# Kernel tuning notes

Hardware: AMD Instinct MI355X
Metric: run time of the kernel (lower is better)

## Reference

```python
import jax, jax.numpy as jnp
import numpy as np

B, NP, PS, D = 4, 512, 16, 1024
NH = 4            # intra attention heads
HD = D // NH      # intra head dim
PH = 4            # pool heads
PHD = D // PH     # pool head dim
K = 5             # depthwise conv kernel size


def _rms_norm(x):
    # F.rms_norm with eps=None -> eps = finfo(dtype).eps, no learned weight
    eps = jnp.finfo(x.dtype).eps
    return x * jax.lax.rsqrt(jnp.mean(x * x, axis=-1, keepdims=True) + eps)


def setup_inputs() -> dict:
    key = jax.random.key(0)
    ks = jax.random.split(key, 12)
    s = 0.02
    return {
        "patch_byte_emb": jax.random.normal(ks[0], (B, NP, PS, D), jnp.float32),
        "local_pos": jax.random.normal(ks[1], (PS, D), jnp.float32) * 0.01,
        "w_gate": jax.random.normal(ks[2], (D, D), jnp.float32) * s,
        "w_in": jax.random.normal(ks[3], (D, D), jnp.float32) * s,
        "conv_w": jax.random.normal(ks[4], (D, 1, K), jnp.float32) * s,  # depthwise (out=D, in/groups=1, k)
        "w_qkv": jax.random.normal(ks[5], (3 * D, D), jnp.float32) * s,
        "w_intra_out": jax.random.normal(ks[6], (D, D), jnp.float32) * s,
        "w_pool": jax.random.normal(ks[7], (PH, D), jnp.float32) * s,
        "attn_temperature": jnp.ones((1,), jnp.float32),
        "w_up": jax.random.normal(ks[8], (D, D), jnp.float32) * s,
        "w_down": jax.random.normal(ks[9], (D, D), jnp.float32) * s,
        "w_out": jax.random.normal(ks[10], (D, D), jnp.float32) * s,
    }


def reference(patch_byte_emb, local_pos, w_gate, w_in, conv_w, w_qkv,
              w_intra_out, w_pool, attn_temperature, w_up, w_down, w_out):
    x = patch_byte_emb + local_pos[None, None]            # [B,NP,PS,D]
    x = _rms_norm(x)
    # SiLU-gated projection (CastedLinear: y = x @ W.T, no bias)
    x = jax.nn.silu(x @ w_gate.T) * (x @ w_in.T)
    bsz, num_patches, patch_size, model_dim = x.shape

    # depthwise causal-style conv1d: padding=4 both sides, then keep first PS outputs
    x_flat = x.reshape(bsz * num_patches, patch_size, model_dim).transpose(0, 2, 1)  # [BN,D,PS]
    conv_out = jax.lax.conv_general_dilated(
        x_flat, conv_w, window_strides=(1,), padding=[(K - 1, K - 1)],
        feature_group_count=model_dim,
        dimension_numbers=("NCH", "OIH", "NCH"))[:, :, :patch_size]
    x = x + conv_out.transpose(0, 2, 1).reshape(bsz, num_patches, patch_size, model_dim)

    # tiny per-patch self-attention
    x_sa = _rms_norm(x).reshape(bsz * num_patches, patch_size, model_dim)
    qkv = (x_sa @ w_qkv.T).reshape(bsz * num_patches, patch_size, 3, NH, HD)
    q, k, v = qkv[:, :, 0], qkv[:, :, 1], qkv[:, :, 2]    # [BN,PS,NH,HD]
    attn = jnp.einsum("bqhd,bkhd->bhqk", q, k) * (HD ** -0.5)
    attn = jax.nn.softmax(attn, axis=-1)
    sa = jnp.einsum("bhqk,bkhd->bqhd", attn, v).reshape(bsz * num_patches, patch_size, model_dim)
    x = x + (sa @ w_intra_out.T).reshape(bsz, num_patches, patch_size, model_dim)

    # multi-head attention pooling over patch positions
    x = _rms_norm(x)
    temp = jnp.clip(attn_temperature, 0.01, None).astype(x.dtype)  # [1]
    attn_logits = (x @ w_pool.T) / temp                   # [B,NP,PS,PH]
    attn_w = jax.nn.softmax(attn_logits.transpose(0, 1, 3, 2), axis=-1)  # [B,NP,PH,PS]
    x_heads = x.reshape(bsz, num_patches, patch_size, PH, PHD)
    pooled = jnp.einsum("bnhp,bnphd->bnhd", attn_w, x_heads).reshape(bsz, num_patches, model_dim)

    # post MLP + out proj
    y = pooled + (jax.nn.silu(_rms_norm(pooled) @ w_up.T) @ w_down.T)
    y = y @ w_out.T
    return _rms_norm(y)
```

## Files before the change

### kernel.cpp

```cpp
#include <hip/hip_runtime.h>
#include <cstdint>
#include <cstddef>


typedef __bf16 bf16x8 __attribute__((ext_vector_type(8)));
typedef float floatx4 __attribute__((ext_vector_type(4)));

#define DEV static __device__ __forceinline__

DEV unsigned short f2bf(float f) {
  union { float f; unsigned u; } x; x.f = f;
  unsigned r = x.u + 0x7fffu + ((x.u >> 16) & 1u);
  return (unsigned short)(r >> 16);
}
DEV float bf2f(unsigned short b) {
  union { unsigned u; float f; } x; x.u = ((unsigned)b) << 16;
  return x.f;
}
DEV float silu_f(float v) { return v / (1.f + __expf(-v)); }

DEV void gl_lds16(const unsigned short* g, unsigned short* l) {
  __builtin_amdgcn_global_load_lds(
      (const __attribute__((address_space(1))) void*)g,
      (__attribute__((address_space(3))) void*)l, 16, 0, 0);
}

DEV float block_reduce_sum(float v) {
  #pragma unroll
  for (int o = 32; o > 0; o >>= 1) v += __shfl_down(v, o, 64);
  __shared__ float s[4];
  int w = threadIdx.x >> 6;
  if ((threadIdx.x & 63) == 0) s[w] = v;
  __syncthreads();
  return s[0] + s[1] + s[2] + s[3];
}

struct CvtArgs {
  const float* src[7];
  unsigned short* dst[7];
  int blkoff[8];
};
__global__ __launch_bounds__(256) void cvt_all(CvtArgs a) {
  int b = blockIdx.x;
  int w = 0;
  #pragma unroll
  for (int i = 0; i < 6; i++) w += (b >= a.blkoff[i + 1]) ? 1 : 0;
  int i = (b - a.blkoff[w]) * 1024 + threadIdx.x * 4;
  float4 v = *(const float4*)(a.src[w] + i);
  ushort4 o;
  o.x = f2bf(v.x); o.y = f2bf(v.y); o.z = f2bf(v.z); o.w = f2bf(v.w);
  *(ushort4*)(a.dst[w] + i) = o;
}

__global__ __launch_bounds__(256) void prep_kernel(const float* __restrict__ pbe,
                                                   const float* __restrict__ pos,
                                                   unsigned short* __restrict__ xn) {
  int row = blockIdx.x;
  int t = row & 15;
  const float* ip = pbe + (size_t)row * 1024;
  const float* pp = pos + (size_t)t * 1024;
  int c = threadIdx.x * 4;
  float4 v = *(const float4*)(ip + c);
  float4 p = *(const float4*)(pp + c);
  v.x += p.x; v.y += p.y; v.z += p.z; v.w += p.w;
  float ss = v.x * v.x + v.y * v.y + v.z * v.z + v.w * v.w;
  ss = block_reduce_sum(ss);
  float sc = rsqrtf(ss * (1.f / 1024.f) + 1.1920929e-7f);
  ushort4 o;
  o.x = f2bf(v.x * sc); o.y = f2bf(v.y * sc); o.z = f2bf(v.z * sc); o.w = f2bf(v.w * sc);
  *(ushort4*)(xn + (size_t)row * 1024 + c) = o;
}

DEV float ldval(const float* p, size_t i) { return p[i]; }
DEV float ldval(const unsigned short* p, size_t i) { return bf2f(p[i]); }
DEV void stval(float* p, size_t i, float v) { p[i] = v; }
DEV void stval(unsigned short* p, size_t i, float v) { p[i] = f2bf(v); }

template <typename TI, typename TO>
__global__ __launch_bounds__(256) void rmsnorm_kernel(const TI* __restrict__ in,
                                                      TO* __restrict__ out) {
  size_t row = blockIdx.x;
  const TI* ip = in + row * 1024;
  TO* op = out + row * 1024;
  int c = threadIdx.x * 4;
  float v[4]; float ss = 0.f;
  #pragma unroll
  for (int j = 0; j < 4; j++) { v[j] = ldval(ip, c + j); ss += v[j] * v[j]; }
  ss = block_reduce_sum(ss);
  float sc = rsqrtf(ss * (1.f / 1024.f) + 1.1920929e-7f);
  #pragma unroll
  for (int j = 0; j < 4; j++) stval(op, c + j, v[j] * sc);
}


DEV void stage_tile(const unsigned short* __restrict__ src, size_t ld,
                    unsigned short* lds, int wave, int lane, int k0) {
  int r0 = wave * 32 + (lane >> 2);
  int r1 = r0 + 16;
  int c0 = (lane & 3) ^ ((r0 >> 1) & 3);
  int c1 = (lane & 3) ^ ((r1 >> 1) & 3);
  gl_lds16(src + (size_t)r0 * ld + k0 + c0 * 8, lds + wave * 1024);
  gl_lds16(src + (size_t)r1 * ld + k0 + c1 * 8, lds + wave * 1024 + 512);
}
DEV void stage_tile64(const unsigned short* __restrict__ src, size_t ld,
                      unsigned short* lds, int wave, int lane, int k0) {
  int r = wave * 16 + (lane >> 2);
  int c = (lane & 3) ^ ((r >> 1) & 3);
  gl_lds16(src + (size_t)r * ld + k0 + c * 8, lds + wave * 512);
}
DEV int frag_off(int row, int quad) {
  return row * 32 + ((quad ^ ((row >> 1) & 3)) * 8);
}

template <int EPI>
__global__ __launch_bounds__(256) void gemm_bt(
    const unsigned short* __restrict__ A, const unsigned short* __restrict__ Bw,
    int M, int N, int K,
    float* __restrict__ outF, unsigned short* __restrict__ outB,
    const unsigned short* __restrict__ resB, const float* __restrict__ resF) {
  __shared__ __align__(16) unsigned short As[128 * 32];
  __shared__ __align__(16) unsigned short Bs[128 * 32];
  const int tid = threadIdx.x;
  const int bm = blockIdx.y * 128, bn = blockIdx.x * 128;
  const int wave = tid >> 6, lane = tid & 63;
  const int wy = wave >> 1, wx = wave & 1;
  const int l15 = lane & 15, quad = lane >> 4;

  floatx4 acc[4][4];
  #pragma unroll
  for (int i = 0; i < 4; i++)
    #pragma unroll
    for (int j = 0; j < 4; j++)
      #pragma unroll
      for (int r = 0; r < 4; r++) acc[i][j][r] = 0.f;

  const unsigned short* Ab = A + (size_t)bm * K;
  const unsigned short* Bb = Bw + (size_t)bn * K;
  int aoff[4], boff[4];
  #pragma unroll
  for (int i = 0; i < 4; i++) {
    aoff[i] = frag_off(wy * 64 + i * 16 + l15, quad);
    boff[i] = frag_off(wx * 64 + i * 16 + l15, quad);
  }

  for (int k0 = 0; k0 < K; k0 += 32) {
    __syncthreads();
    stage_tile(Ab, K, As, wave, lane, k0);
    stage_tile(Bb, K, Bs, wave, lane, k0);
    __syncthreads();
    bf16x8 afr[4], bfr[4];
    #pragma unroll
    for (int i = 0; i < 4; i++) afr[i] = *(const bf16x8*)&As[aoff[i]];
    #pragma unroll
    for (int j = 0; j < 4; j++) bfr[j] = *(const bf16x8*)&Bs[boff[j]];
    #pragma unroll
    for (int i = 0; i < 4; i++)
      #pragma unroll
      for (int j = 0; j < 4; j++)
        acc[i][j] = __builtin_amdgcn_mfma_f32_16x16x32_bf16(afr[i], bfr[j], acc[i][j], 0, 0, 0);
  }

  #pragma unroll
  for (int i = 0; i < 4; i++)
    #pragma unroll
    for (int j = 0; j < 4; j++) {
      int gm = bm + wy * 64 + i * 16 + quad * 4;
      int gn = bn + wx * 64 + j * 16 + l15;
      #pragma unroll
      for (int r = 0; r < 4; r++) {
        float v = acc[i][j][r];
        size_t idx = (size_t)(gm + r) * N + gn;
        if (EPI == 0) outF[idx] = v;
        else if (EPI == 1) outB[idx] = f2bf(v);
        else if (EPI == 2) outB[idx] = f2bf(silu_f(v));
        else if (EPI == 3) outB[idx] = f2bf(v + bf2f(resB[idx]));
        else if (EPI == 4) outB[idx] = f2bf(v + resF[idx]);
      }
    }
}

__global__ __launch_bounds__(256, 2) void gemm_dual(
    const unsigned short* __restrict__ A, const unsigned short* __restrict__ Bg,
    const unsigned short* __restrict__ Bi, int M, int N, int K,
    unsigned short* __restrict__ outH) {
  __shared__ __align__(16) unsigned short As[128 * 32];
  __shared__ __align__(16) unsigned short Gs[64 * 32];
  __shared__ __align__(16) unsigned short Is[64 * 32];
  const int tid = threadIdx.x;
  const int bm = blockIdx.y * 128, bn = blockIdx.x * 64;
  const int wave = tid >> 6, lane = tid & 63;
  const int wy = wave >> 1, wx = wave & 1;
  const int l15 = lane & 15, quad = lane >> 4;

  floatx4 accg[4][2], acci[4][2];
  #pragma unroll
  for (int i = 0; i < 4; i++)
    #pragma unroll
    for (int j = 0; j < 2; j++)
      #pragma unroll
      for (int r = 0; r < 4; r++) { accg[i][j][r] = 0.f; acci[i][j][r] = 0.f; }

  const unsigned short* Ab = A + (size_t)bm * K;
  const unsigned short* Gb = Bg + (size_t)bn * K;
  const unsigned short* Ib = Bi + (size_t)bn * K;
  int aoff[4], boff[2];
  #pragma unroll
  for (int i = 0; i < 4; i++) aoff[i] = frag_off(wy * 64 + i * 16 + l15, quad);
  #pragma unroll
  for (int j = 0; j < 2; j++) boff[j] = frag_off(wx * 32 + j * 16 + l15, quad);

  for (int k0 = 0; k0 < K; k0 += 32) {
    __syncthreads();
    stage_tile(Ab, K, As, wave, lane, k0);
    stage_tile64(Gb, K, Gs, wave, lane, k0);
    stage_tile64(Ib, K, Is, wave, lane, k0);
    __syncthreads();
    bf16x8 afr[4], gfr[2], ifr[2];
    #pragma unroll
    for (int i = 0; i < 4; i++) afr[i] = *(const bf16x8*)&As[aoff[i]];
    #pragma unroll
    for (int j = 0; j < 2; j++) {
      gfr[j] = *(const bf16x8*)&Gs[boff[j]];
      ifr[j] = *(const bf16x8*)&Is[boff[j]];
    }
    #pragma unroll
    for (int i = 0; i < 4; i++)
      #pragma unroll
      for (int j = 0; j < 2; j++) {
        accg[i][j] = __builtin_amdgcn_mfma_f32_16x16x32_bf16(afr[i], gfr[j], accg[i][j], 0, 0, 0);
        acci[i][j] = __builtin_amdgcn_mfma_f32_16x16x32_bf16(afr[i], ifr[j], acci[i][j], 0, 0, 0);
      }
  }

  #pragma unroll
  for (int i = 0; i < 4; i++)
    #pragma unroll
    for (int j = 0; j < 2; j++) {
      int gm = bm + wy * 64 + i * 16 + quad * 4;
      int gn = bn + wx * 32 + j * 16 + l15;
      #pragma unroll
      for (int r = 0; r < 4; r++) {
        size_t idx = (size_t)(gm + r) * N + gn;
        outH[idx] = f2bf(silu_f(accg[i][j][r]) * acci[i][j][r]);
      }
    }
}

__global__ __launch_bounds__(256) void conv_rms_kernel(const unsigned short* __restrict__ h,
                                                       const float* __restrict__ cw,
                                                       unsigned short* __restrict__ x2,
                                                       unsigned short* __restrict__ x2n) {
  int patch = blockIdx.x;
  __shared__ __align__(16) unsigned short hs[16 * 1024];
  __shared__ __align__(16) float cws[5120];
  const int tid = threadIdx.x;
  size_t base = (size_t)patch * 16384;
  for (int idx = tid * 8; idx < 16384; idx += 256 * 8)
    *(uint4*)&hs[idx] = *(const uint4*)&h[base + idx];
  for (int i = tid * 4; i < 5120; i += 256 * 4)
    *(float4*)&cws[i] = *(const float4*)&cw[i];
  __syncthreads();
  int t = tid >> 4;
  int lc = (tid & 15) * 8;
  float vals[8][8];
  float ss = 0.f;
  #pragma unroll
  for (int jb = 0; jb < 8; jb++) {
    #pragma unroll
    for (int i = 0; i < 8; i++) {
      int c = jb * 128 + lc + i;
      float acc = bf2f(hs[t * 1024 + c]);
      #pragma unroll
      for (int k = 0; k < 5; k++) {
        int tt = t + k - 4;
        if (tt >= 0) acc += cws[c * 5 + k] * bf2f(hs[tt * 1024 + c]);
      }
      vals[jb][i] = acc;
      ss += acc * acc;
    }
  }
  ss += __shfl_down(ss, 8, 16);
  ss += __shfl_down(ss, 4, 16);
  ss += __shfl_down(ss, 2, 16);
  ss += __shfl_down(ss, 1, 16);
  ss = __shfl(ss, 0, 16);
  float sc = rsqrtf(ss * (1.f / 1024.f) + 1.1920929e-7f);
  #pragma unroll
  for (int jb = 0; jb < 8; jb++) {
    ushort4 o2[2], on[2];
    #pragma unroll
    for (int i = 0; i < 8; i++) {
      ((unsigned short*)o2)[i] = f2bf(vals[jb][i]);
      ((unsigned short*)on)[i] = f2bf(vals[jb][i] * sc);
    }
    size_t off = base + (size_t)t * 1024 + jb * 128 + lc;
    *(uint4*)&x2[off] = *(uint4*)o2;
    *(uint4*)&x2n[off] = *(uint4*)on;
  }
}

__global__ __launch_bounds__(256) void attn_kernel(const unsigned short* __restrict__ qkv,
                                                   unsigned short* __restrict__ sa) {
  int patch = blockIdx.x;
  int head = blockIdx.y;
  const int tid = threadIdx.x;
  __shared__ float qs[16][260], ks[16][260], vs[16][260];
  __shared__ float sc[16][16];
  size_t base = (size_t)patch * 16 * 3072 + (size_t)head * 256;
  for (int idx = tid * 8; idx < 16 * 256; idx += 256 * 8) {
    int t = idx >> 8, d = idx & 255;
    size_t roff = base + (size_t)t * 3072 + d;
    uint4 qv = *(const uint4*)&qkv[roff];
    uint4 kv = *(const uint4*)&qkv[roff + 1024];
    uint4 vv = *(const uint4*)&qkv[roff + 2048];
    const unsigned short* qp = (const unsigned short*)&qv;
    const unsigned short* kp = (const unsigned short*)&kv;
    const unsigned short* vp = (const unsigned short*)&vv;
    #pragma unroll
    for (int i = 0; i < 8; i++) {
      qs[t][d + i] = bf2f(qp[i]);
      ks[t][d + i] = bf2f(kp[i]);
      vs[t][d + i] = bf2f(vp[i]);
    }
  }
  __syncthreads();
  {
    int t = tid >> 4, kk = tid & 15;
    float s = 0.f;
    for (int d = 0; d < 256; d++) s += qs[t][d] * ks[kk][d];
    sc[t][kk] = s * 0.0625f;
  }
  __syncthreads();
  if (tid < 16) {
    float m = -1e30f;
    for (int kk = 0; kk < 16; kk++) m = fmaxf(m, sc[tid][kk]);
    float p[16], sum = 0.f;
    for (int kk = 0; kk < 16; kk++) { p[kk] = __expf(sc[tid][kk] - m); sum += p[kk]; }
    float inv = 1.f / sum;
    for (int kk = 0; kk < 16; kk++) sc[tid][kk] = p[kk] * inv;
  }
  __syncthreads();
  for (int idx = tid * 8; idx < 4096; idx += 256 * 8) {
    int t = idx >> 8, d = idx & 255;
    ushort4 o[2];
    #pragma unroll
    for (int i = 0; i < 8; i++) {
      float v = 0.f;
      #pragma unroll
      for (int kk = 0; kk < 16; kk++) v += sc[t][kk] * vs[kk][d + i];
      ((unsigned short*)o)[i] = f2bf(v);
    }
    *(uint4*)&sa[(size_t)(patch * 16 + t) * 1024 + head * 256 + d] = *(uint4*)o;
  }
}

__global__ __launch_bounds__(256) void pool_kernel(const unsigned short* __restrict__ x4,
                                                   const float* __restrict__ wpool,
                                                   const float* __restrict__ tptr,
                                                   float* __restrict__ pooled) {
  int patch = blockIdx.x;
  __shared__ __align__(16) unsigned short xs[16 * 1024];
  __shared__ float lg[4][16], aw[4][16];
  const int tid = threadIdx.x;
  size_t base = (size_t)patch * 16384;
  for (int idx = tid * 8; idx < 16384; idx += 256 * 8)
    *(uint4*)&xs[idx] = *(const uint4*)&x4[base + idx];
  __syncthreads();
  {
    int pair = tid >> 2, sub = tid & 3;
    int t = pair >> 2, hh = pair & 3;
    float s = 0.f;
    for (int d = sub * 256; d < sub * 256 + 256; d++)
      s += bf2f(xs[t * 1024 + d]) * wpool[hh * 1024 + d];
    s += __shfl_down(s, 2, 64);
    s += __shfl_down(s, 1, 64);
    if (sub == 0) {
      float temp = fmaxf(tptr[0], 0.01f);
      lg[hh][t] = s / temp;
    }
  }
  __syncthreads();
  if (tid < 4) {
    int hh = tid;
    float m = -1e30f;
    for (int t = 0; t < 16; t++) m = fmaxf(m, lg[hh][t]);
    float p[16], sum = 0.f;
    for (int t = 0; t < 16; t++) { p[t] = __expf(lg[hh][t] - m); sum += p[t]; }
    float inv = 1.f / sum;
    for (int t = 0; t < 16; t++) aw[hh][t] = p[t] * inv;
  }
  __syncthreads();
  for (int c = tid; c < 1024; c += 256) {
    int hh = c >> 8;
    float o = 0.f;
    #pragma unroll
    for (int t = 0; t < 16; t++) o += aw[hh][t] * bf2f(xs[t * 1024 + c]);
    pooled[(size_t)patch * 1024 + c] = o;
  }
}

extern "C" void kernel_launch(void* const* d_in, const int* in_sizes, int n_in,
                              void* d_out, int out_size, void* d_ws, size_t ws_size,
                              hipStream_t stream) {
  (void)in_sizes; (void)n_in; (void)out_size; (void)ws_size;
  const float* pbe  = (const float*)d_in[0];
  const float* lpos = (const float*)d_in[1];
  const float* wg   = (const float*)d_in[2];
  const float* wi   = (const float*)d_in[3];
  const float* cw   = (const float*)d_in[4];
  const float* wqkv = (const float*)d_in[5];
  const float* wio  = (const float*)d_in[6];
  const float* wpl  = (const float*)d_in[7];
  const float* temp = (const float*)d_in[8];
  const float* wup  = (const float*)d_in[9];
  const float* wdn  = (const float*)d_in[10];
  const float* wout = (const float*)d_in[11];
  float* outp = (float*)d_out;

  const int ROWS = 32768, Dm = 1024, NPAT = 2048;

  char* p = (char*)d_ws;
  auto take = [&](size_t nbytes) { void* r = (void*)p; p += (nbytes + 255) & ~(size_t)255; return r; };
  unsigned short* wg_b   = (unsigned short*)take((size_t)Dm * Dm * 2);
  unsigned short* wi_b   = (unsigned short*)take((size_t)Dm * Dm * 2);
  unsigned short* wqkv_b = (unsigned short*)take((size_t)3 * Dm * Dm * 2);
  unsigned short* wio_b  = (unsigned short*)take((size_t)Dm * Dm * 2);
  unsigned short* wup_b  = (unsigned short*)take((size_t)Dm * Dm * 2);
  unsigned short* wdn_b  = (unsigned short*)take((size_t)Dm * Dm * 2);
  unsigned short* wout_b = (unsigned short*)take((size_t)Dm * Dm * 2);
  unsigned short* slotA  = (unsigned short*)take((size_t)ROWS * Dm * 2);
  unsigned short* slotB  = (unsigned short*)take((size_t)ROWS * Dm * 2);
  unsigned short* slotC  = (unsigned short*)take((size_t)ROWS * Dm * 2);
  unsigned short* qkvB   = (unsigned short*)take((size_t)ROWS * 3 * Dm * 2);
  float*          pooled = (float*)take((size_t)NPAT * Dm * 4);
  unsigned short* pooledn= (unsigned short*)take((size_t)NPAT * Dm * 2);
  unsigned short* ubuf   = (unsigned short*)take((size_t)NPAT * Dm * 2);
  unsigned short* y1b    = (unsigned short*)take((size_t)NPAT * Dm * 2);
  float*          y2     = (float*)take((size_t)NPAT * Dm * 4);

  CvtArgs ca;
  ca.src[0] = wg;   ca.dst[0] = wg_b;
  ca.src[1] = wi;   ca.dst[1] = wi_b;
  ca.src[2] = wqkv; ca.dst[2] = wqkv_b;
  ca.src[3] = wio;  ca.dst[3] = wio_b;
  ca.src[4] = wup;  ca.dst[4] = wup_b;
  ca.src[5] = wdn;  ca.dst[5] = wdn_b;
  ca.src[6] = wout; ca.dst[6] = wout_b;
  int off = 0;
  for (int i = 0; i < 7; i++) { ca.blkoff[i] = off; off += (i == 2) ? 3072 : 1024; }
  ca.blkoff[7] = off;
  cvt_all<<<dim3(off), dim3(256), 0, stream>>>(ca);

  prep_kernel<<<dim3(ROWS), dim3(256), 0, stream>>>(pbe, lpos, slotA);
  gemm_dual<<<dim3(Dm / 64, ROWS / 128), dim3(256), 0, stream>>>(
      slotA, wg_b, wi_b, ROWS, Dm, Dm, slotB);
  conv_rms_kernel<<<dim3(NPAT), dim3(256), 0, stream>>>(slotB, cw, slotC, slotA);
  gemm_bt<1><<<dim3(3 * Dm / 128, ROWS / 128), dim3(256), 0, stream>>>(
      slotA, wqkv_b, ROWS, 3 * Dm, Dm, nullptr, qkvB, nullptr, nullptr);
  attn_kernel<<<dim3(NPAT, 4), dim3(256), 0, stream>>>(qkvB, slotB);
  gemm_bt<3><<<dim3(Dm / 128, ROWS / 128), dim3(256), 0, stream>>>(
      slotB, wio_b, ROWS, Dm, Dm, nullptr, slotC, slotC, nullptr);
  rmsnorm_kernel<unsigned short, unsigned short><<<dim3(ROWS), dim3(256), 0, stream>>>(slotC, slotA);
  pool_kernel<<<dim3(NPAT), dim3(256), 0, stream>>>(slotA, wpl, temp, pooled);
  rmsnorm_kernel<float, unsigned short><<<dim3(NPAT), dim3(256), 0, stream>>>(pooled, pooledn);
  gemm_bt<2><<<dim3(Dm / 128, NPAT / 128), dim3(256), 0, stream>>>(
      pooledn, wup_b, NPAT, Dm, Dm, nullptr, ubuf, nullptr, nullptr);
  gemm_bt<4><<<dim3(Dm / 128, NPAT / 128), dim3(256), 0, stream>>>(
      ubuf, wdn_b, NPAT, Dm, Dm, nullptr, y1b, nullptr, pooled);
  gemm_bt<0><<<dim3(Dm / 128, NPAT / 128), dim3(256), 0, stream>>>(
      y1b, wout_b, NPAT, Dm, Dm, y2, nullptr, nullptr, nullptr);
  rmsnorm_kernel<float, float><<<dim3(NPAT), dim3(256), 0, stream>>>(y2, outp);
}
```

Baseline: 1.179 ms.

## Deepen GEMM K-tiles to 64, vectorize conv/attention, fuse pooled rmsnorm

```diff
diff --git a/kernel.cpp b/kernel.cpp
--- a/kernel.cpp
+++ b/kernel.cpp
@@ -93,79 +93,80 @@
 }
 
 
-DEV void stage_tile(const unsigned short* __restrict__ src, size_t ld,
-                    unsigned short* lds, int wave, int lane, int k0) {
-  int r0 = wave * 32 + (lane >> 2);
-  int r1 = r0 + 16;
-  int c0 = (lane & 3) ^ ((r0 >> 1) & 3);
-  int c1 = (lane & 3) ^ ((r1 >> 1) & 3);
-  gl_lds16(src + (size_t)r0 * ld + k0 + c0 * 8, lds + wave * 1024);
-  gl_lds16(src + (size_t)r1 * ld + k0 + c1 * 8, lds + wave * 1024 + 512);
-}
-DEV void stage_tile64(const unsigned short* __restrict__ src, size_t ld,
-                      unsigned short* lds, int wave, int lane, int k0) {
-  int r = wave * 16 + (lane >> 2);
-  int c = (lane & 3) ^ ((r >> 1) & 3);
-  gl_lds16(src + (size_t)r * ld + k0 + c * 8, lds + wave * 512);
-}
-DEV int frag_off(int row, int quad) {
-  return row * 32 + ((quad ^ ((row >> 1) & 3)) * 8);
-}
-
-template <int EPI>
+template <int R>
+DEV void stage_rows(const unsigned short* __restrict__ src, int ldK,
+                    unsigned short* lds, int k0, int wave, int lane) {
+  constexpr int PER_WAVE = R / 32;
+  #pragma unroll
+  for (int d = 0; d < PER_WAVE; d++) {
+    int di = wave * PER_WAVE + d;
+    int r = di * 8 + (lane >> 3);
+    int c = (lane & 7) ^ (r & 7);
+    gl_lds16(src + (size_t)r * ldK + k0 + c * 8, lds + di * 512);
+  }
+}
+DEV int frag_off64(int row, int g) {
+  return row * 64 + ((g ^ (row & 7)) * 8);
+}
+
+template <int EPI, int TM, int TN>
 __global__ __launch_bounds__(256) void gemm_bt(
     const unsigned short* __restrict__ A, const unsigned short* __restrict__ Bw,
     int M, int N, int K,
     float* __restrict__ outF, unsigned short* __restrict__ outB,
     const unsigned short* __restrict__ resB, const float* __restrict__ resF) {
-  __shared__ __align__(16) unsigned short As[128 * 32];
-  __shared__ __align__(16) unsigned short Bs[128 * 32];
+  constexpr int AI = TM / 32;
+  constexpr int BJ = TN / 32;
+  __shared__ __align__(16) unsigned short As[TM * 64];
+  __shared__ __align__(16) unsigned short Bs[TN * 64];
   const int tid = threadIdx.x;
-  const int bm = blockIdx.y * 128, bn = blockIdx.x * 128;
+  const int bm = blockIdx.y * TM, bn = blockIdx.x * TN;
   const int wave = tid >> 6, lane = tid & 63;
   const int wy = wave >> 1, wx = wave & 1;
   const int l15 = lane & 15, quad = lane >> 4;
 
-  floatx4 acc[4][4];
-  #pragma unroll
-  for (int i = 0; i < 4; i++)
-    #pragma unroll
-    for (int j = 0; j < 4; j++)
+  floatx4 acc[AI][BJ];
+  #pragma unroll
+  for (int i = 0; i < AI; i++)
+    #pragma unroll
+    for (int j = 0; j < BJ; j++)
       #pragma unroll
       for (int r = 0; r < 4; r++) acc[i][j][r] = 0.f;
 
   const unsigned short* Ab = A + (size_t)bm * K;
   const unsigned short* Bb = Bw + (size_t)bn * K;
-  int aoff[4], boff[4];
-  #pragma unroll
-  for (int i = 0; i < 4; i++) {
-    aoff[i] = frag_off(wy * 64 + i * 16 + l15, quad);
-    boff[i] = frag_off(wx * 64 + i * 16 + l15, quad);
-  }
-
-  for (int k0 = 0; k0 < K; k0 += 32) {
+  int arow[AI], brow[BJ];
+  #pragma unroll
+  for (int i = 0; i < AI; i++) arow[i] = wy * (TM / 2) + i * 16 + l15;
+  #pragma unroll
+  for (int j = 0; j < BJ; j++) brow[j] = wx * (TN / 2) + j * 16 + l15;
+
+  for (int k0 = 0; k0 < K; k0 += 64) {
     __syncthreads();
-    stage_tile(Ab, K, As, wave, lane, k0);
-    stage_tile(Bb, K, Bs, wave, lane, k0);
+    stage_rows<TM>(Ab, K, As, k0, wave, lane);
+    stage_rows<TN>(Bb, K, Bs, k0, wave, lane);
     __syncthreads();
-    bf16x8 afr[4], bfr[4];
-    #pragma unroll
-    for (int i = 0; i < 4; i++) afr[i] = *(const bf16x8*)&As[aoff[i]];
-    #pragma unroll
-    for (int j = 0; j < 4; j++) bfr[j] = *(const bf16x8*)&Bs[boff[j]];
-    #pragma unroll
-    for (int i = 0; i < 4; i++)
-      #pragma unroll
-      for (int j = 0; j < 4; j++)
-        acc[i][j] = __builtin_amdgcn_mfma_f32_16x16x32_bf16(afr[i], bfr[j], acc[i][j], 0, 0, 0);
-  }
-
-  #pragma unroll
-  for (int i = 0; i < 4; i++)
-    #pragma unroll
-    for (int j = 0; j < 4; j++) {
-      int gm = bm + wy * 64 + i * 16 + quad * 4;
-      int gn = bn + wx * 64 + j * 16 + l15;
+    #pragma unroll
+    for (int h = 0; h < 2; h++) {
+      bf16x8 afr[AI], bfr[BJ];
+      #pragma unroll
+      for (int i = 0; i < AI; i++) afr[i] = *(const bf16x8*)&As[frag_off64(arow[i], h * 4 + quad)];
+      #pragma unroll
+      for (int j = 0; j < BJ; j++) bfr[j] = *(const bf16x8*)&Bs[frag_off64(brow[j], h * 4 + quad)];
+      #pragma unroll
+      for (int i = 0; i < AI; i++)
+        #pragma unroll
+        for (int j = 0; j < BJ; j++)
+          acc[i][j] = __builtin_amdgcn_mfma_f32_16x16x32_bf16(afr[i], bfr[j], acc[i][j], 0, 0, 0);
+    }
+  }
+
+  #pragma unroll
+  for (int i = 0; i < AI; i++)
+    #pragma unroll
+    for (int j = 0; j < BJ; j++) {
+      int gm = bm + wy * (TM / 2) + i * 16 + quad * 4;
+      int gn = bn + wx * (TN / 2) + j * 16 + l15;
       #pragma unroll
       for (int r = 0; r < 4; r++) {
         float v = acc[i][j][r];
@@ -179,13 +180,13 @@
     }
 }
 
-__global__ __launch_bounds__(256, 2) void gemm_dual(
+__global__ __launch_bounds__(256) void gemm_dual(
     const unsigned short* __restrict__ A, const unsigned short* __restrict__ Bg,
     const unsigned short* __restrict__ Bi, int M, int N, int K,
     unsigned short* __restrict__ outH) {
-  __shared__ __align__(16) unsigned short As[128 * 32];
-  __shared__ __align__(16) unsigned short Gs[64 * 32];
-  __shared__ __align__(16) unsigned short Is[64 * 32];
+  __shared__ __align__(16) unsigned short As[128 * 64];
+  __shared__ __align__(16) unsigned short Gs[64 * 64];
+  __shared__ __align__(16) unsigned short Is[64 * 64];
   const int tid = threadIdx.x;
   const int bm = blockIdx.y * 128, bn = blockIdx.x * 64;
   const int wave = tid >> 6, lane = tid & 63;
@@ -203,33 +204,36 @@
   const unsigned short* Ab = A + (size_t)bm * K;
   const unsigned short* Gb = Bg + (size_t)bn * K;
   const unsigned short* Ib = Bi + (size_t)bn * K;
-  int aoff[4], boff[2];
-  #pragma unroll
-  for (int i = 0; i < 4; i++) aoff[i] = frag_off(wy * 64 + i * 16 + l15, quad);
-  #pragma unroll
-  for (int j = 0; j < 2; j++) boff[j] = frag_off(wx * 32 + j * 16 + l15, quad);
-
-  for (int k0 = 0; k0 < K; k0 += 32) {
+  int arow[4], brow[2];
+  #pragma unroll
+  for (int i = 0; i < 4; i++) arow[i] = wy * 64 + i * 16 + l15;
+  #pragma unroll
+  for (int j = 0; j < 2; j++) brow[j] = wx * 32 + j * 16 + l15;
+
+  for (int k0 = 0; k0 < K; k0 += 64) {
     __syncthreads();
-    stage_tile(Ab, K, As, wave, lane, k0);
-    stage_tile64(Gb, K, Gs, wave, lane, k0);
-    stage_tile64(Ib, K, Is, wave, lane, k0);
+    stage_rows<128>(Ab, K, As, k0, wave, lane);
+    stage_rows<64>(Gb, K, Gs, k0, wave, lane);
+    stage_rows<64>(Ib, K, Is, k0, wave, lane);
     __syncthreads();
-    bf16x8 afr[4], gfr[2], ifr[2];
-    #pragma unroll
-    for (int i = 0; i < 4; i++) afr[i] = *(const bf16x8*)&As[aoff[i]];
-    #pragma unroll
-    for (int j = 0; j < 2; j++) {
-      gfr[j] = *(const bf16x8*)&Gs[boff[j]];
-      ifr[j] = *(const bf16x8*)&Is[boff[j]];
-    }
-    #pragma unroll
-    for (int i = 0; i < 4; i++)
+    #pragma unroll
+    for (int h = 0; h < 2; h++) {
+      bf16x8 afr[4], gfr[2], ifr[2];
+      #pragma unroll
+      for (int i = 0; i < 4; i++) afr[i] = *(const bf16x8*)&As[frag_off64(arow[i], h * 4 + quad)];
       #pragma unroll
       for (int j = 0; j < 2; j++) {
-        accg[i][j] = __builtin_amdgcn_mfma_f32_16x16x32_bf16(afr[i], gfr[j], accg[i][j], 0, 0, 0);
-        acci[i][j] = __builtin_amdgcn_mfma_f32_16x16x32_bf16(afr[i], ifr[j], acci[i][j], 0, 0, 0);
+        gfr[j] = *(const bf16x8*)&Gs[frag_off64(brow[j], h * 4 + quad)];
+        ifr[j] = *(const bf16x8*)&Is[frag_off64(brow[j], h * 4 + quad)];
       }
+      #pragma unroll
+      for (int i = 0; i < 4; i++)
+        #pragma unroll
+        for (int j = 0; j < 2; j++) {
+          accg[i][j] = __builtin_amdgcn_mfma_f32_16x16x32_bf16(afr[i], gfr[j], accg[i][j], 0, 0, 0);
+          acci[i][j] = __builtin_amdgcn_mfma_f32_16x16x32_bf16(afr[i], ifr[j], acci[i][j], 0, 0, 0);
+        }
+    }
   }
 
   #pragma unroll
@@ -246,19 +250,24 @@
     }
 }
 
+#define HS_LD 1040
 __global__ __launch_bounds__(256) void conv_rms_kernel(const unsigned short* __restrict__ h,
                                                        const float* __restrict__ cw,
                                                        unsigned short* __restrict__ x2,
                                                        unsigned short* __restrict__ x2n) {
   int patch = blockIdx.x;
-  __shared__ __align__(16) unsigned short hs[16 * 1024];
-  __shared__ __align__(16) float cws[5120];
+  __shared__ __align__(16) unsigned short hs[16 * HS_LD];
+  __shared__ __align__(16) float cwp[5 * 1024];
   const int tid = threadIdx.x;
   size_t base = (size_t)patch * 16384;
-  for (int idx = tid * 8; idx < 16384; idx += 256 * 8)
-    *(uint4*)&hs[idx] = *(const uint4*)&h[base + idx];
-  for (int i = tid * 4; i < 5120; i += 256 * 4)
-    *(float4*)&cws[i] = *(const float4*)&cw[i];
+  for (int idx = tid * 8; idx < 16384; idx += 256 * 8) {
+    int row = idx >> 10, col = idx & 1023;
+    *(uint4*)&hs[row * HS_LD + col] = *(const uint4*)&h[base + idx];
+  }
+  for (int i = tid; i < 5120; i += 256) {
+    int c = i / 5, k = i - c * 5;
+    cwp[k * 1024 + c] = cw[i];
+  }
   __syncthreads();
   int t = tid >> 4;
   int lc = (tid & 15) * 8;
@@ -266,15 +275,34 @@
   float ss = 0.f;
   #pragma unroll
   for (int jb = 0; jb < 8; jb++) {
+    int c = jb * 128 + lc;
+    float tap[5][8];
+    #pragma unroll
+    for (int k = 0; k < 5; k++) {
+      int tt = t + k - 4;
+      if (tt >= 0) {
+        uint4 v = *(const uint4*)&hs[tt * HS_LD + c];
+        const unsigned short* vp = (const unsigned short*)&v;
+        #pragma unroll
+        for (int i = 0; i < 8; i++) tap[k][i] = bf2f(vp[i]);
+      } else {
+        #pragma unroll
+        for (int i = 0; i < 8; i++) tap[k][i] = 0.f;
+      }
+    }
+    float w[5][8];
+    #pragma unroll
+    for (int k = 0; k < 5; k++) {
+      float4 a = *(const float4*)&cwp[k * 1024 + c];
+      float4 b = *(const float4*)&cwp[k * 1024 + c + 4];
+      w[k][0] = a.x; w[k][1] = a.y; w[k][2] = a.z; w[k][3] = a.w;
+      w[k][4] = b.x; w[k][5] = b.y; w[k][6] = b.z; w[k][7] = b.w;
+    }
     #pragma unroll
     for (int i = 0; i < 8; i++) {
-      int c = jb * 128 + lc + i;
-      float acc = bf2f(hs[t * 1024 + c]);
-      #pragma unroll
-      for (int k = 0; k < 5; k++) {
-        int tt = t + k - 4;
-        if (tt >= 0) acc += cws[c * 5 + k] * bf2f(hs[tt * 1024 + c]);
-      }
+      float acc = tap[4][i];
+      #pragma unroll
+      for (int k = 0; k < 5; k++) acc += w[k][i] * tap[k][i];
       vals[jb][i] = acc;
       ss += acc * acc;
     }
@@ -327,7 +355,11 @@
   {
     int t = tid >> 4, kk = tid & 15;
     float s = 0.f;
-    for (int d = 0; d < 256; d++) s += qs[t][d] * ks[kk][d];
+    for (int d = 0; d < 256; d += 4) {
+      float4 q = *(const float4*)&qs[t][d];
+      float4 k = *(const float4*)&ks[kk][d];
+      s += q.x * k.x + q.y * k.y + q.z * k.z + q.w * k.w;
+    }
     sc[t][kk] = s * 0.0625f;
   }
   __syncthreads();
@@ -342,22 +374,27 @@
   __syncthreads();
   for (int idx = tid * 8; idx < 4096; idx += 256 * 8) {
     int t = idx >> 8, d = idx & 255;
-    ushort4 o[2];
-    #pragma unroll
-    for (int i = 0; i < 8; i++) {
-      float v = 0.f;
-      #pragma unroll
-      for (int kk = 0; kk < 16; kk++) v += sc[t][kk] * vs[kk][d + i];
-      ((unsigned short*)o)[i] = f2bf(v);
-    }
-    *(uint4*)&sa[(size_t)(patch * 16 + t) * 1024 + head * 256 + d] = *(uint4*)o;
+    float o[8] = {0, 0, 0, 0, 0, 0, 0, 0};
+    #pragma unroll
+    for (int kk = 0; kk < 16; kk++) {
+      float w = sc[t][kk];
+      float4 v0 = *(const float4*)&vs[kk][d];
+      float4 v1 = *(const float4*)&vs[kk][d + 4];
+      o[0] += w * v0.x; o[1] += w * v0.y; o[2] += w * v0.z; o[3] += w * v0.w;
+      o[4] += w * v1.x; o[5] += w * v1.y; o[6] += w * v1.z; o[7] += w * v1.w;
+    }
+    ushort4 ov[2];
+    #pragma unroll
+    for (int i = 0; i < 8; i++) ((unsigned short*)ov)[i] = f2bf(o[i]);
+    *(uint4*)&sa[(size_t)(patch * 16 + t) * 1024 + head * 256 + d] = *(uint4*)ov;
   }
 }
 
 __global__ __launch_bounds__(256) void pool_kernel(const unsigned short* __restrict__ x4,
                                                    const float* __restrict__ wpool,
                                                    const float* __restrict__ tptr,
-                                                   float* __restrict__ pooled) {
+                                                   float* __restrict__ pooled,
+                                                   unsigned short* __restrict__ pooledn) {
   int patch = blockIdx.x;
   __shared__ __align__(16) unsigned short xs[16 * 1024];
   __shared__ float lg[4][16], aw[4][16];
@@ -390,12 +427,24 @@
     for (int t = 0; t < 16; t++) aw[hh][t] = p[t] * inv;
   }
   __syncthreads();
-  for (int c = tid; c < 1024; c += 256) {
+  float ov[4]; int cs[4];
+  float ss = 0.f;
+  #pragma unroll
+  for (int q = 0; q < 4; q++) {
+    int c = tid + q * 256;
     int hh = c >> 8;
     float o = 0.f;
     #pragma unroll
     for (int t = 0; t < 16; t++) o += aw[hh][t] * bf2f(xs[t * 1024 + c]);
-    pooled[(size_t)patch * 1024 + c] = o;
+    ov[q] = o; cs[q] = c;
+    ss += o * o;
+  }
+  ss = block_reduce_sum(ss);
+  float scn = rsqrtf(ss * (1.f / 1024.f) + 1.1920929e-7f);
+  #pragma unroll
+  for (int q = 0; q < 4; q++) {
+    pooled[(size_t)patch * 1024 + cs[q]] = ov[q];
+    pooledn[(size_t)patch * 1024 + cs[q]] = f2bf(ov[q] * scn);
   }
 }
 
@@ -455,19 +504,18 @@
   gemm_dual<<<dim3(Dm / 64, ROWS / 128), dim3(256), 0, stream>>>(
       slotA, wg_b, wi_b, ROWS, Dm, Dm, slotB);
   conv_rms_kernel<<<dim3(NPAT), dim3(256), 0, stream>>>(slotB, cw, slotC, slotA);
-  gemm_bt<1><<<dim3(3 * Dm / 128, ROWS / 128), dim3(256), 0, stream>>>(
+  gemm_bt<1, 128, 128><<<dim3(3 * Dm / 128, ROWS / 128), dim3(256), 0, stream>>>(
       slotA, wqkv_b, ROWS, 3 * Dm, Dm, nullptr, qkvB, nullptr, nullptr);
   attn_kernel<<<dim3(NPAT, 4), dim3(256), 0, stream>>>(qkvB, slotB);
-  gemm_bt<3><<<dim3(Dm / 128, ROWS / 128), dim3(256), 0, stream>>>(
+  gemm_bt<3, 128, 128><<<dim3(Dm / 128, ROWS / 128), dim3(256), 0, stream>>>(
       slotB, wio_b, ROWS, Dm, Dm, nullptr, slotC, slotC, nullptr);
   rmsnorm_kernel<unsigned short, unsigned short><<<dim3(ROWS), dim3(256), 0, stream>>>(slotC, slotA);
-  pool_kernel<<<dim3(NPAT), dim3(256), 0, stream>>>(slotA, wpl, temp, pooled);
-  rmsnorm_kernel<float, unsigned short><<<dim3(NPAT), dim3(256), 0, stream>>>(pooled, pooledn);
-  gemm_bt<2><<<dim3(Dm / 128, NPAT / 128), dim3(256), 0, stream>>>(
+  pool_kernel<<<dim3(NPAT), dim3(256), 0, stream>>>(slotA, wpl, temp, pooled, pooledn);
+  gemm_bt<2, 64, 128><<<dim3(Dm / 128, NPAT / 64), dim3(256), 0, stream>>>(
       pooledn, wup_b, NPAT, Dm, Dm, nullptr, ubuf, nullptr, nullptr);
-  gemm_bt<4><<<dim3(Dm / 128, NPAT / 128), dim3(256), 0, stream>>>(
+  gemm_bt<4, 64, 128><<<dim3(Dm / 128, NPAT / 64), dim3(256), 0, stream>>>(
       ubuf, wdn_b, NPAT, Dm, Dm, nullptr, y1b, nullptr, pooled);
-  gemm_bt<0><<<dim3(Dm / 128, NPAT / 128), dim3(256), 0, stream>>>(
+  gemm_bt<0, 64, 128><<<dim3(Dm / 128, NPAT / 64), dim3(256), 0, stream>>>(
       y1b, wout_b, NPAT, Dm, Dm, y2, nullptr, nullptr, nullptr);
   rmsnorm_kernel<float, float><<<dim3(NPAT), dim3(256), 0, stream>>>(y2, outp);
 }
```

New measurement: 1.141 ms. 3.2% less time.
